# Kernel tuning notes

Measured on AMD Instinct MI355X. Metric: run time of the kernel, lower is better.

Reference implementation:

```python
import jax, jax.numpy as jnp
import numpy as np

N_INPUT, N_HIDDEN, N_LAYERS = 256, 1024, 3
BATCH, SEQ = 32, 512


def _uniform(key, shape, std):
    return jax.random.uniform(key, shape, jnp.float32, -std, std)


def setup_inputs() -> dict:
    key = jax.random.key(0)
    keys = jax.random.split(key, 32)
    std = 1.0 / float(np.sqrt(N_HIDDEN))
    inp = {"inputs": jax.random.normal(keys[0], (BATCH, SEQ, N_INPUT), jnp.float32)}
    ki = 1
    for l in range(N_LAYERS):
        d_in = N_INPUT if l == 0 else N_HIDDEN
        inp[f"Wxh{l}"] = _uniform(keys[ki], (3 * N_HIDDEN, d_in), std); ki += 1
        inp[f"bxh{l}"] = _uniform(keys[ki], (3 * N_HIDDEN,), std); ki += 1
        inp[f"Whh{l}"] = _uniform(keys[ki], (3 * N_HIDDEN, N_HIDDEN), std); ki += 1
        inp[f"bhh{l}"] = _uniform(keys[ki], (3 * N_HIDDEN,), std); ki += 1
        inp[f"Wnh{l}"] = _uniform(keys[ki], (3 * N_HIDDEN, N_INPUT), std); ki += 1
        inp[f"bnh{l}"] = _uniform(keys[ki], (3 * N_HIDDEN,), std); ki += 1
    inp["Wout"] = _uniform(keys[ki], (N_INPUT, N_HIDDEN), std); ki += 1
    inp["bout"] = _uniform(keys[ki], (N_INPUT,), std)
    return inp


def _moving_mean(x, s):
    # x: [T, B, D] -> sliding-window mean over time, window s, stride 1 -> [T-s+1, B, D]
    if s == 1:
        return x
    T = x.shape[0]
    return jnp.mean(jnp.stack([x[i:T - s + 1 + i] for i in range(s)], axis=0), axis=0)


def _gru_layer(xs, ms, h0, Wxh, bxh, Whh, bhh, Wnh, bnh):
    # xs, ms: [Tm, B, d] aligned per-timestep; h0: [B, H]
    # Precompute the time-parallel input/ms projections (batched GEMM).
    gx = jnp.einsum('tbd,gd->tbg', xs, Wxh) + bxh   # [Tm, B, 3H]
    gn = jnp.einsum('tbd,gd->tbg', ms, Wnh) + bnh   # [Tm, B, 3H]

    def step(h, g):
        gxt, gnt = g
        gh = h @ Whh.T + bhh
        i_r, i_i, i_n = jnp.split(gxt, 3, axis=-1)
        h_r, h_i, h_n = jnp.split(gh, 3, axis=-1)
        n_r, n_i, n_n = jnp.split(gnt, 3, axis=-1)
        resetgate = jax.nn.sigmoid(i_r + h_r + n_r)
        inputgate = jax.nn.sigmoid(i_i + h_i + n_i)
        newgate = jnp.tanh(i_n + resetgate * h_n + n_n)
        h_new = newgate + inputgate * (h - newgate)
        return h_new, h_new

    h_last, outs = jax.lax.scan(step, h0, (gx, gn))
    return outs, h_last


def reference(inputs,
              Wxh0, bxh0, Whh0, bhh0, Wnh0, bnh0,
              Wxh1, bxh1, Whh1, bhh1, Wnh1, bnh1,
              Wxh2, bxh2, Whh2, bhh2, Wnh2, bnh2,
              Wout, bout):
    params = [(Wxh0, bxh0, Whh0, bhh0, Wnh0, bnh0),
              (Wxh1, bxh1, Whh1, bhh1, Wnh1, bnh1),
              (Wxh2, bxh2, Whh2, bhh2, Wnh2, bnh2)]
    x = jnp.transpose(inputs, (1, 0, 2))  # batch_first -> [T, B, D]
    ms_list = [_moving_mean(x, 2 ** l) for l in range(N_LAYERS)]
    layer_in = x
    layers, hiddens = [], []
    for l in range(N_LAYERS):
        ms = ms_list[l]
        Tm = ms.shape[0]
        xs = layer_in[layer_in.shape[0] - Tm:]  # align tail of previous layer output
        h0 = jnp.zeros((x.shape[1], N_HIDDEN), dtype=x.dtype)
        outs, h_last = _gru_layer(xs, ms, h0, *params[l])
        layers.append(outs)
        hiddens.append(h_last)
        layer_in = outs
    layers = [jnp.einsum('tbh,oh->tbo', y, Wout) + bout for y in layers]
    return (*layers, *hiddens)
```

## Files before the change

### kernel.cpp

```cpp
#include <hip/hip_runtime.h>
#include <hip/hip_bf16.h>

typedef __bf16 bf16;
typedef __bf16 bf16x8 __attribute__((ext_vector_type(8)));
typedef float floatx4 __attribute__((ext_vector_type(4)));
typedef float floatx2 __attribute__((ext_vector_type(2)));
typedef unsigned int uint;
typedef uint uintx4 __attribute__((ext_vector_type(4)));
typedef unsigned long long u64;
typedef u64 u64x2 __attribute__((ext_vector_type(2)));
typedef __attribute__((address_space(1))) void gvoid;
typedef __attribute__((address_space(3))) void lvoid;

#define MFMA16(a, b, c) __builtin_amdgcn_mfma_f32_16x16x32_bf16((a), (b), (c), 0, 0, 0)
#define NB_REC 64
#define NB_W 64
#define FLAG_STRIDE 32
#define HSTR 1040
#define CHUNKF (32 * 32 * 3072)
#define AG __ATOMIC_RELAXED, __HIP_MEMORY_SCOPE_AGENT

struct MegaArgs {
    const bf16* xs[3];  int lda[3];
    const bf16* wXh[3]; int nkx[3];
    const bf16* ms[3];
    const bf16* wNh[3];
    const float* bxh[3]; const float* bnh[3];
    const float* Whh[3]; const float* bhh[3];
    bf16* outs[3];
    float* hid[3];
    float* G[3];
    uint* bar[3];
    uint* cdone[3];
    bf16* h01[3];
    int T[3];
};

static __device__ __forceinline__ floatx2 ldg2(const float* p) {
    union { u64 q; floatx2 f; } u;
    u.q = __hip_atomic_load((const u64*)p, AG);
    return u.f;
}

__global__ void k_cvt(const float* __restrict__ src, bf16* __restrict__ dst, int n) {
    int idx = blockIdx.x * 256 + threadIdx.x;
    if (idx < n) dst[idx] = (bf16)src[idx];
}

__global__ void k_prep(const float* __restrict__ inp, bf16* __restrict__ xT,
                       uint* __restrict__ bar) {
    size_t idx = (size_t)blockIdx.x * 256 + threadIdx.x;
    if (blockIdx.x == 0) {
        for (int i = threadIdx.x; i < 3 * NB_REC * FLAG_STRIDE + 64; i += 256)
            bar[i] = 0;
    }
    int d = (int)(idx & 255);
    int t = (int)((idx >> 8) & 511);
    int b = (int)(idx >> 17);
    xT[((size_t)(t * 32 + b) << 8) | d] = (bf16)inp[idx];
}

__global__ void k_movmean(const bf16* __restrict__ xT, bf16* __restrict__ out,
                          int s) {
    size_t idx = (size_t)blockIdx.x * 256 + threadIdx.x;
    int d = (int)(idx & 255);
    int m = (int)(idx >> 8);
    int t = m >> 5, b = m & 31;
    float acc = 0.f;
    for (int i = 0; i < s; ++i)
        acc += (float)xT[(((size_t)(t + i) * 32 + b) << 8) | d];
    out[idx] = (bf16)(acc * (1.f / (float)s));
}

__global__ __launch_bounds__(256, 2) void k_gemm(
    const bf16* __restrict__ A1, int lda1, const bf16* __restrict__ W1, int nk1,
    const bf16* __restrict__ A2, int lda2, const bf16* __restrict__ W2, int nk2,
    const float* __restrict__ bias1, const float* __restrict__ bias2,
    float* __restrict__ Cf, bf16* __restrict__ Cb, int ldc, int Mstore) {
    __shared__ bf16 lsA[128 * 64];
    __shared__ bf16 lsW[128 * 64];
    const int tid = threadIdx.x;
    const int lane = tid & 63, w = tid >> 6;
    const int quad = lane >> 4, lr = lane & 15;
    const int wm = w >> 1, wn = w & 1;
    const int m0 = blockIdx.y * 128, n0 = blockIdx.x * 128;

    floatx4 acc[4][4] = {};
    const bf16* As[2] = {A1, A2};
    const bf16* Ws[2] = {W1, W2};
    const int ldas[2] = {lda1, lda2};
    const int nks[2] = {nk1, nk2};

    for (int ph = 0; ph < 2; ++ph) {
        const int nk = nks[ph];
        if (nk == 0) continue;
        const bf16* A = As[ph];
        const bf16* Wp = Ws[ph];
        const int lda = ldas[ph];
        const int ldw = nk * 64;
        for (int kb = 0; kb < nk; ++kb) {
            const bf16* Ab = A + (size_t)m0 * lda + (size_t)kb * 64;
            const bf16* Wb = Wp + (size_t)n0 * ldw + (size_t)kb * 64;
#pragma unroll
            for (int i = 0; i < 4; ++i) {
                int c = (i * 4 + w) * 64 + lane;
                int m = c >> 3, q = c & 7;
                const bf16* g1 = Ab + (size_t)m * lda + ((q ^ (m & 7)) << 3);
                __builtin_amdgcn_global_load_lds((const gvoid*)g1,
                                                 (lvoid*)(lsA + (i * 4 + w) * 512), 16, 0, 0);
                const bf16* g2 = Wb + (size_t)m * ldw + ((q ^ (m & 7)) << 3);
                __builtin_amdgcn_global_load_lds((const gvoid*)g2,
                                                 (lvoid*)(lsW + (i * 4 + w) * 512), 16, 0, 0);
            }
            __syncthreads();
#pragma unroll
            for (int s = 0; s < 2; ++s) {
                bf16x8 af[4], bfr[4];
#pragma unroll
                for (int i = 0; i < 4; ++i) {
                    int kc = s * 4 + quad;
                    int m = wm * 64 + i * 16 + lr;
                    af[i] = *(const bf16x8*)(lsA + m * 64 + ((kc ^ (m & 7)) << 3));
                    int n = wn * 64 + i * 16 + lr;
                    bfr[i] = *(const bf16x8*)(lsW + n * 64 + ((kc ^ (n & 7)) << 3));
                }
#pragma unroll
                for (int i = 0; i < 4; ++i)
#pragma unroll
                    for (int j = 0; j < 4; ++j)
                        acc[i][j] = MFMA16(af[i], bfr[j], acc[i][j]);
            }
            __syncthreads();
        }
    }
#pragma unroll
    for (int j = 0; j < 4; ++j) {
        int col = n0 + wn * 64 + j * 16 + lr;
        float bs = 0.f;
        if (bias1) bs += bias1[col];
        if (bias2) bs += bias2[col];
#pragma unroll
        for (int i = 0; i < 4; ++i) {
            int rowb = m0 + wm * 64 + i * 16 + quad * 4;
#pragma unroll
            for (int r = 0; r < 4; ++r) {
                int row = rowb + r;
                if (row < Mstore) {
                    float v = acc[i][j][r] + bs;
                    if (Cf) Cf[(size_t)row * ldc + col] = v;
                    else    Cb[(size_t)row * ldc + col] = (bf16)v;
                }
            }
        }
    }
}

__global__ __launch_bounds__(384, 1) void k_rec(
    const float* __restrict__ G, const float* __restrict__ Whh,
    const float* __restrict__ bhh, bf16* __restrict__ outs,
    bf16* __restrict__ h01, float* __restrict__ hf,
    float* __restrict__ hid_out, uint* __restrict__ bar,
    int T, int init, int final_, uint tgt0) {
    const int tid = threadIdx.x, blk = blockIdx.x;
    const int lane = tid & 63, w = tid >> 6;
    const int quad = lane >> 4, lr = lane & 15;
    const int mi = (w >= 3) ? 1 : 0, ni = w - mi * 3;

    __shared__ __attribute__((aligned(16))) char smem[73088];
    bf16* hT = (bf16*)smem;
    float* gh = (float*)(smem + 66560);

    const float* wrow = Whh + ((size_t)ni * 1024 + blk * 16 + lr) * 1024 + quad * 8;
    bf16x8 breg[32];
#pragma unroll
    for (int kt = 0; kt < 32; ++kt) {
        const floatx4* p = (const floatx4*)(wrow + kt * 32);
        floatx4 lo = p[0], hi = p[1];
        bf16x8 b;
        b[0] = (bf16)lo.x; b[1] = (bf16)lo.y; b[2] = (bf16)lo.z; b[3] = (bf16)lo.w;
        b[4] = (bf16)hi.x; b[5] = (bf16)hi.y; b[6] = (bf16)hi.z; b[7] = (bf16)hi.w;
        breg[kt] = b;
    }

    const int eb = tid >> 3;
    const int ec = (tid & 7) * 2;
    const int ecg = blk * 16 + ec;

    float bhr0 = 0.f, bhr1 = 0.f, bhi0 = 0.f, bhi1 = 0.f, bhn0 = 0.f, bhn1 = 0.f;
    float hreg0 = 0.f, hreg1 = 0.f;
    if (tid < 256) {
        bhr0 = bhh[ecg];        bhr1 = bhh[ecg + 1];
        bhi0 = bhh[1024 + ecg]; bhi1 = bhh[1024 + ecg + 1];
        bhn0 = bhh[2048 + ecg]; bhn1 = bhh[2048 + ecg + 1];
        if (!init) {
            floatx2 h = *(const floatx2*)(hf + (size_t)eb * 1024 + ecg);
            hreg0 = h.x;
            hreg1 = h.y;
        }
        union { bf16 h[2]; uint u; } pk;
        pk.h[0] = (bf16)hreg0;
        pk.h[1] = (bf16)hreg1;
        __hip_atomic_store((uint*)(h01 + (size_t)eb * 1024 + ecg), pk.u, AG);
    }

    floatx2 pAr, pAi, pAn, pBr, pBi, pBn;
    if (tid < 256) {
        const float* Grow = G + (size_t)eb * 3072 + ecg;
        pAr = *(const floatx2*)(Grow);
        pAi = *(const floatx2*)(Grow + 1024);
        pAn = *(const floatx2*)(Grow + 2048);
    }

    uint* myflag = bar + (uint)blk * FLAG_STRIDE;

    __syncthreads();
    if (tid == 0) __hip_atomic_store(myflag, tgt0, AG);
    if (tid < NB_REC) {
        const uint* fp = bar + (uint)tid * FLAG_STRIDE;
        while (__hip_atomic_load(fp, AG) < tgt0) __builtin_amdgcn_s_sleep(1);
    }
    __syncthreads();

    for (int t = 0; t < T; ++t) {
        const bf16* hb = h01 + (size_t)(t & 1) * (32 * 1024);
        bf16* hn = h01 + (size_t)((t + 1) & 1) * (32 * 1024);

        u64 s0[11], s1[11];
#pragma unroll
        for (int r = 0; r < 11; ++r) {
            int ci = tid + r * 384;
            if (r < 10 || ci < 4096) {
                const u64* src = (const u64*)(hb + (size_t)ci * 8);
                s0[r] = __hip_atomic_load(src, AG);
                s1[r] = __hip_atomic_load(src + 1, AG);
            }
        }
#pragma unroll
        for (int r = 0; r < 11; ++r) {
            int ci = tid + r * 384;
            if (r < 10 || ci < 4096) {
                int row = ci >> 7, q = ci & 127;
                u64x2 v; v.x = s0[r]; v.y = s1[r];
                *(u64x2*)(hT + row * HSTR + q * 8) = v;
            }
        }
        __syncthreads();

        floatx4 acc0 = {0.f, 0.f, 0.f, 0.f}, acc1 = {0.f, 0.f, 0.f, 0.f};
        const bf16* aB = hT + (mi * 16 + lr) * HSTR + quad * 8;
#pragma unroll
        for (int kt = 0; kt < 32; kt += 2) {
            bf16x8 a0 = *(const bf16x8*)(aB + kt * 32);
            acc0 = MFMA16(a0, breg[kt], acc0);
            bf16x8 a1 = *(const bf16x8*)(aB + kt * 32 + 32);
            acc1 = MFMA16(a1, breg[kt + 1], acc1);
        }
        floatx4 acc = acc0 + acc1;
#pragma unroll
        for (int r = 0; r < 4; ++r)
            gh[(ni * 32 + mi * 16 + quad * 4 + r) * 17 + lr] = acc[r];
        __syncthreads();

        uint pku = 0u;
        if (tid < 256) {
            float ghr0 = gh[eb * 17 + ec]            + bhr0;
            float ghr1 = gh[eb * 17 + ec + 1]        + bhr1;
            float ghi0 = gh[(32 + eb) * 17 + ec]     + bhi0;
            float ghi1 = gh[(32 + eb) * 17 + ec + 1] + bhi1;
            float ghn0 = gh[(64 + eb) * 17 + ec]     + bhn0;
            float ghn1 = gh[(64 + eb) * 17 + ec + 1] + bhn1;
            float rg0 = 1.f / (1.f + __expf(-(pAr.x + ghr0)));
            float rg1 = 1.f / (1.f + __expf(-(pAr.y + ghr1)));
            float ig0 = 1.f / (1.f + __expf(-(pAi.x + ghi0)));
            float ig1 = 1.f / (1.f + __expf(-(pAi.y + ghi1)));
            float pre0 = pAn.x + rg0 * ghn0;
            float pre1 = pAn.y + rg1 * ghn1;
            float e20 = __expf(2.f * pre0);
            float e21 = __expf(2.f * pre1);
            float ng0 = 1.f - 2.f / (e20 + 1.f);
            float ng1 = 1.f - 2.f / (e21 + 1.f);
            hreg0 = ng0 + ig0 * (hreg0 - ng0);
            hreg1 = ng1 + ig1 * (hreg1 - ng1);
            union { bf16 h[2]; uint u; } pk;
            pk.h[0] = (bf16)hreg0;
            pk.h[1] = (bf16)hreg1;
            pku = pk.u;
            __hip_atomic_store((uint*)(hn + (size_t)eb * 1024 + ecg), pku, AG);
        }
        __syncthreads();

        uint tgt = tgt0 + 1 + (uint)t;
        if (tid == 0) __hip_atomic_store(myflag, tgt, AG);

        if (tid < 256) {
            if (t + 1 < T) {
                const float* Grow = G + ((size_t)(t + 1) * 32 + eb) * 3072 + ecg;
                pBr = *(const floatx2*)(Grow);
                pBi = *(const floatx2*)(Grow + 1024);
                pBn = *(const floatx2*)(Grow + 2048);
            }
            *(uint*)(outs + ((size_t)t * 32 + eb) * 1024 + ecg) = pku;
        }
        if (t + 1 < T && tid < NB_REC) {
            const uint* fp = bar + (uint)tid * FLAG_STRIDE;
            while (__hip_atomic_load(fp, AG) < tgt) __builtin_amdgcn_s_sleep(1);
        }
        __syncthreads();

        pAr = pBr; pAi = pBi; pAn = pBn;
    }

    if (tid < 256) {
        floatx2 h; h.x = hreg0; h.y = hreg1;
        *(floatx2*)(hf + (size_t)eb * 1024 + ecg) = h;
        if (final_) *(floatx2*)(hid_out + (size_t)eb * 1024 + ecg) = h;
    }
}

__global__ __launch_bounds__(384, 1) void k_mega(MegaArgs A) {
    __shared__ __attribute__((aligned(16))) char smem[98304];
    const int tid = threadIdx.x, blk = blockIdx.x;
    const int lane = tid & 63, w = tid >> 6;
    const int quad = lane >> 4, lr = lane & 15;

    if (blk >= 192) {
        bf16* lsA = (bf16*)smem;
        bf16* lsW = (bf16*)(smem + 16384);
        const int wid = blk - 192;
        const int wr = w / 3, wc = w - wr * 3;
        for (int key = 0; key <= 36; ++key) {
            for (int l = 0; l < 3; ++l) {
                int rem = key - 3 * l;
                if (rem < 0 || (rem & 1)) continue;
                int c = rem >> 1;
                if (c >= 16) continue;
                if (l > 0) {
                    uint need = (uint)((c + 1) * 32 + l + 1);
                    uint cap = (uint)(A.T[l - 1] + 2);
                    if (need > cap) need = cap;
                    if (tid < 64) {
                        const uint* fp = A.bar[l - 1] + (uint)tid * FLAG_STRIDE;
                        while (__hip_atomic_load(fp, AG) < need)
                            __builtin_amdgcn_s_sleep(2);
                    }
                }
                if (c >= 2) {
                    uint need = (uint)((c - 1) * 32);
                    if (tid < 64) {
                        const uint* fp = A.bar[l] + (uint)tid * FLAG_STRIDE;
                        while (__hip_atomic_load(fp, AG) < need)
                            __builtin_amdgcn_s_sleep(2);
                    }
                }
                __syncthreads();
                const bf16* xsP = A.xs[l];
                const bf16* msP = A.ms[l];
                const bf16* wxP = A.wXh[l];
                const bf16* wnP = A.wNh[l];
                const float* b1 = A.bxh[l];
                const float* b2 = A.bnh[l];
                float* Gs = A.G[l] + (size_t)(c & 1) * CHUNKF;
                const int Mst = A.T[l] * 32;
                const int nks[2] = {A.nkx[l], 4};
                const bf16* Aps[2] = {xsP, msP};
                const int ldas[2] = {A.lda[l], 256};
                const bf16* Wps[2] = {wxP, wnP};
#pragma unroll 1
                for (int half = 0; half < 2; ++half) {
                    int tl = wid * 2 + half;
                    int by = tl >> 4, bx = tl & 15;
                    int m0g = c * 1024 + by * 128;
                    int n0 = bx * 192;
                    floatx4 acc[4][4] = {};
                    for (int ph = 0; ph < 2; ++ph) {
                        const int nk = nks[ph];
                        const bf16* Ap = Aps[ph];
                        const int ldap = ldas[ph];
                        const bf16* Wp = Wps[ph];
                        const int ldw = nk * 64;
                        for (int kb = 0; kb < nk; ++kb) {
                            const bf16* Ab = Ap + (size_t)m0g * ldap + (size_t)kb * 64;
                            const bf16* Wb = Wp + (size_t)n0 * ldw + (size_t)kb * 64;
#pragma unroll
                            for (int r = 0; r < 7; ++r) {
                                int idx = tid + r * 384;
                                if (r < 6 || idx < 2560) {
                                    if (idx < 1024) {
                                        int m = idx >> 3, q = idx & 7;
                                        const bf16* src = Ab + (size_t)m * ldap + ((q ^ (m & 7)) << 3);
                                        __builtin_amdgcn_global_load_lds(
                                            (const gvoid*)src, (lvoid*)(lsA + idx * 8), 16, 0, 0);
                                    } else {
                                        int j2 = idx - 1024;
                                        int m = j2 >> 3, q = j2 & 7;
                                        const bf16* src = Wb + (size_t)m * ldw + ((q ^ (m & 7)) << 3);
                                        __builtin_amdgcn_global_load_lds(
                                            (const gvoid*)src, (lvoid*)(lsW + j2 * 8), 16, 0, 0);
                                    }
                                }
                            }
                            __syncthreads();
#pragma unroll
                            for (int s = 0; s < 2; ++s) {
                                bf16x8 af[4], bfr[4];
#pragma unroll
                                for (int i = 0; i < 4; ++i) {
                                    int kc = s * 4 + quad;
                                    int mA = wr * 64 + i * 16 + lr;
                                    af[i] = *(const bf16x8*)(lsA + mA * 64 + ((kc ^ (mA & 7)) << 3));
                                    int nB = wc * 64 + i * 16 + lr;
                                    bfr[i] = *(const bf16x8*)(lsW + nB * 64 + ((kc ^ (nB & 7)) << 3));
                                }
#pragma unroll
                                for (int i = 0; i < 4; ++i)
#pragma unroll
                                    for (int j = 0; j < 4; ++j)
                                        acc[i][j] = MFMA16(af[i], bfr[j], acc[i][j]);
                            }
                            __syncthreads();
                        }
                    }
#pragma unroll
                    for (int j = 0; j < 4; ++j) {
                        int col = n0 + wc * 64 + j * 16 + lr;
                        float bs = b1[col] + b2[col];
#pragma unroll
                        for (int i = 0; i < 4; ++i) {
                            int rowb = m0g + wr * 64 + i * 16 + quad * 4;
#pragma unroll
                            for (int r = 0; r < 4; ++r) {
                                int row = rowb + r;
                                if (row < Mst) {
                                    float v = acc[i][j][r] + bs;
                                    __hip_atomic_store(
                                        (uint*)(Gs + (size_t)(row - c * 1024) * 3072 + col),
                                        __float_as_uint(v), AG);
                                }
                            }
                        }
                    }
                }
                __syncthreads();
                if (tid == 0) atomicAdd(A.cdone[l] + c, 1u);
            }
        }
        return;
    }

    const int l = blk >> 6, cs = blk & 63;
    const int T = A.T[l];
    bf16* hT = (bf16*)smem;
    float* gh = (float*)(smem + 66560);
    const int mi = (w >= 3) ? 1 : 0, ni = w - mi * 3;

    const float* Whh = A.Whh[l];
    const float* bhh = A.bhh[l];
    bf16* outs = A.outs[l];
    bf16* h01 = A.h01[l];
    float* Gb = A.G[l];
    uint* bar = A.bar[l];
    const uint* cdone = A.cdone[l];

    const float* wrow = Whh + ((size_t)ni * 1024 + cs * 16 + lr) * 1024 + quad * 8;
    bf16x8 breg[32];
#pragma unroll
    for (int kt = 0; kt < 32; ++kt) {
        const floatx4* p = (const floatx4*)(wrow + kt * 32);
        floatx4 lo = p[0], hi = p[1];
        bf16x8 b;
        b[0] = (bf16)lo.x; b[1] = (bf16)lo.y; b[2] = (bf16)lo.z; b[3] = (bf16)lo.w;
        b[4] = (bf16)hi.x; b[5] = (bf16)hi.y; b[6] = (bf16)hi.z; b[7] = (bf16)hi.w;
        breg[kt] = b;
    }

    const int eb = tid >> 3;
    const int ec = (tid & 7) * 2;
    const int ecg = cs * 16 + ec;

    float bhr0 = 0.f, bhr1 = 0.f, bhi0 = 0.f, bhi1 = 0.f, bhn0 = 0.f, bhn1 = 0.f;
    if (tid < 256) {
        bhr0 = bhh[ecg];        bhr1 = bhh[ecg + 1];
        bhi0 = bhh[1024 + ecg]; bhi1 = bhh[1024 + ecg + 1];
        bhn0 = bhh[2048 + ecg]; bhn1 = bhh[2048 + ecg + 1];
    }
    float hreg0 = 0.f, hreg1 = 0.f;
    floatx2 pAr = {0.f, 0.f}, pAi = {0.f, 0.f}, pAn = {0.f, 0.f};
    floatx2 pBr = {0.f, 0.f}, pBi = {0.f, 0.f}, pBn = {0.f, 0.f};
    uint* myflag = bar + (uint)cs * FLAG_STRIDE;

    for (int t = 0; t < T; ++t) {
        if ((t & 31) == 0) {
            const uint* cd = cdone + (t >> 5);
            if (tid < 64) {
                while (__hip_atomic_load(cd, AG) < (uint)NB_W)
                    __builtin_amdgcn_s_sleep(1);
            }
            __syncthreads();
            if (tid < 256) {
                const float* Grow = Gb + (size_t)((t >> 5) & 1) * CHUNKF
                                      + ((size_t)(t & 31) * 32 + eb) * 3072 + ecg;
                pAr = ldg2(Grow);
                pAi = ldg2(Grow + 1024);
                pAn = ldg2(Grow + 2048);
            }
        }

        if (t == 0) {
            for (int i = tid; i < 4096; i += 384) {
                int row = i >> 7, q = i & 127;
                uintx4 z = {0u, 0u, 0u, 0u};
                *(uintx4*)(hT + row * HSTR + q * 8) = z;
            }
        } else {
            const bf16* hb = h01 + (size_t)(t & 1) * (32 * 1024);
            u64 s0[11], s1[11];
#pragma unroll
            for (int r = 0; r < 11; ++r) {
                int ci = tid + r * 384;
                if (r < 10 || ci < 4096) {
                    const u64* src = (const u64*)(hb + (size_t)ci * 8);
                    s0[r] = __hip_atomic_load(src, AG);
                    s1[r] = __hip_atomic_load(src + 1, AG);
                }
            }
#pragma unroll
            for (int r = 0; r < 11; ++r) {
                int ci = tid + r * 384;
                if (r < 10 || ci < 4096) {
                    int row = ci >> 7, q = ci & 127;
                    u64x2 v; v.x = s0[r]; v.y = s1[r];
                    *(u64x2*)(hT + row * HSTR + q * 8) = v;
                }
            }
        }
        __syncthreads();

        floatx4 acc0 = {0.f, 0.f, 0.f, 0.f}, acc1 = {0.f, 0.f, 0.f, 0.f};
        const bf16* aB = hT + (mi * 16 + lr) * HSTR + quad * 8;
#pragma unroll
        for (int kt = 0; kt < 32; kt += 2) {
            bf16x8 a0 = *(const bf16x8*)(aB + kt * 32);
            acc0 = MFMA16(a0, breg[kt], acc0);
            bf16x8 a1 = *(const bf16x8*)(aB + kt * 32 + 32);
            acc1 = MFMA16(a1, breg[kt + 1], acc1);
        }
        floatx4 acc = acc0 + acc1;
#pragma unroll
        for (int r = 0; r < 4; ++r)
            gh[(ni * 32 + mi * 16 + quad * 4 + r) * 17 + lr] = acc[r];
        __syncthreads();

        uint pku = 0u;
        if (tid < 256) {
            float ghr0 = gh[eb * 17 + ec]            + bhr0;
            float ghr1 = gh[eb * 17 + ec + 1]        + bhr1;
            float ghi0 = gh[(32 + eb) * 17 + ec]     + bhi0;
            float ghi1 = gh[(32 + eb) * 17 + ec + 1] + bhi1;
            float ghn0 = gh[(64 + eb) * 17 + ec]     + bhn0;
            float ghn1 = gh[(64 + eb) * 17 + ec + 1] + bhn1;
            float rg0 = 1.f / (1.f + __expf(-(pAr.x + ghr0)));
            float rg1 = 1.f / (1.f + __expf(-(pAr.y + ghr1)));
            float ig0 = 1.f / (1.f + __expf(-(pAi.x + ghi0)));
            float ig1 = 1.f / (1.f + __expf(-(pAi.y + ghi1)));
            float pre0 = pAn.x + rg0 * ghn0;
            float pre1 = pAn.y + rg1 * ghn1;
            float e20 = __expf(2.f * pre0);
            float e21 = __expf(2.f * pre1);
            float ng0 = 1.f - 2.f / (e20 + 1.f);
            float ng1 = 1.f - 2.f / (e21 + 1.f);
            hreg0 = ng0 + ig0 * (hreg0 - ng0);
            hreg1 = ng1 + ig1 * (hreg1 - ng1);
            union { bf16 h[2]; uint u; } pk;
            pk.h[0] = (bf16)hreg0;
            pk.h[1] = (bf16)hreg1;
            pku = pk.u;
            __hip_atomic_store((uint*)(h01 + (size_t)((t + 1) & 1) * (32 * 1024)
                                       + (size_t)eb * 1024 + ecg), pku, AG);
        }
        __syncthreads();

        if (tid == 0) __hip_atomic_store(myflag, (uint)(t + 1), AG);

        if (tid < 256) {
            if (t + 1 < T && ((t + 1) & 31) != 0) {
                const float* Grow = Gb + (size_t)((t >> 5) & 1) * CHUNKF
                                      + ((size_t)((t + 1) & 31) * 32 + eb) * 3072 + ecg;
                pBr = ldg2(Grow);
                pBi = ldg2(Grow + 1024);
                pBn = ldg2(Grow + 2048);
            }
            __hip_atomic_store((uint*)(outs + ((size_t)t * 32 + eb) * 1024 + ecg),
                               pku, AG);
        }
        if (t + 1 < T && tid < 64) {
            const uint* fp = bar + (uint)tid * FLAG_STRIDE;
            while (__hip_atomic_load(fp, AG) < (uint)(t + 1))
                __builtin_amdgcn_s_sleep(1);
        }
        __syncthreads();

        pAr = pBr; pAi = pBi; pAn = pBn;
    }

    if (tid == 0) __hip_atomic_store(myflag, (uint)(T + 2), AG);
    if (tid < 256) {
        floatx2 h; h.x = hreg0; h.y = hreg1;
        *(floatx2*)(A.hid[l] + (size_t)eb * 1024 + ecg) = h;
    }
}

extern "C" void kernel_launch(void* const* d_in, const int* in_sizes, int n_in,
                              void* d_out, int out_size, void* d_ws, size_t ws_size,
                              hipStream_t stream) {
    const float* inp  = (const float*)d_in[0];
    const float* Wxh0 = (const float*)d_in[1];
    const float* bxh0 = (const float*)d_in[2];
    const float* Whh0 = (const float*)d_in[3];
    const float* bhh0 = (const float*)d_in[4];
    const float* Wnh0 = (const float*)d_in[5];
    const float* bnh0 = (const float*)d_in[6];
    const float* Wxh1 = (const float*)d_in[7];
    const float* bxh1 = (const float*)d_in[8];
    const float* Whh1 = (const float*)d_in[9];
    const float* bhh1 = (const float*)d_in[10];
    const float* Wnh1 = (const float*)d_in[11];
    const float* bnh1 = (const float*)d_in[12];
    const float* Wxh2 = (const float*)d_in[13];
    const float* bxh2 = (const float*)d_in[14];
    const float* Whh2 = (const float*)d_in[15];
    const float* bhh2 = (const float*)d_in[16];
    const float* Wnh2 = (const float*)d_in[17];
    const float* bnh2 = (const float*)d_in[18];
    const float* Wout = (const float*)d_in[19];
    const float* bout = (const float*)d_in[20];
    float* out = (float*)d_out;

    char* ws = (char*)d_ws;
    size_t o = 0;
    auto take = [&](size_t bytes) {
        o = (o + 255) & ~(size_t)255;
        char* p = ws + o;
        o += bytes;
        return p;
    };
    const size_t RP = 16512;
    bf16* xT    = (bf16*)take(RP * 256 * 2);
    bf16* ms1   = (bf16*)take(RP * 256 * 2);
    bf16* ms2   = (bf16*)take(RP * 256 * 2);
    bf16* outs0 = (bf16*)take(RP * 1024 * 2);
    bf16* outs1 = (bf16*)take(RP * 1024 * 2);
    bf16* outs2 = (bf16*)take(RP * 1024 * 2);
    bf16* h01   = (bf16*)take((size_t)3 * 2 * 32 * 1024 * 2);
    float* hf   = (float*)take((size_t)32 * 1024 * 4);
    uint* bar   = (uint*)take((size_t)(3 * NB_REC * FLAG_STRIDE + 64) * 4);
    bf16* wXh0 = (bf16*)take((size_t)3072 * 256 * 2);
    bf16* wXh1 = (bf16*)take((size_t)3072 * 1024 * 2);
    bf16* wXh2 = (bf16*)take((size_t)3072 * 1024 * 2);
    bf16* wNh0 = (bf16*)take((size_t)3072 * 256 * 2);
    bf16* wNh1 = (bf16*)take((size_t)3072 * 256 * 2);
    bf16* wNh2 = (bf16*)take((size_t)3072 * 256 * 2);
    bf16* wOut = (bf16*)take((size_t)256 * 1024 * 2);
    o = (o + 255) & ~(size_t)255;
    float* G = (float*)(ws + o);
    size_t availG = (ws_size > o) ? (ws_size - o) : 0;
    const int use_mega = availG >= (size_t)6 * CHUNKF * 4;
    (void)in_sizes; (void)n_in; (void)out_size;

    const size_t o0 = 0, o1 = (size_t)512 * 32 * 256, o2 = o1 + (size_t)511 * 32 * 256;
    const size_t ohid = o2 + (size_t)509 * 32 * 256;

    auto cvt = [&](const float* s, bf16* d, int n) {
        k_cvt<<<(n + 255) / 256, 256, 0, stream>>>(s, d, n);
    };
    cvt(Wout, wOut, 256 * 1024);
    cvt(Wxh0, wXh0, 3072 * 256);
    cvt(Wxh1, wXh1, 3072 * 1024);
    cvt(Wxh2, wXh2, 3072 * 1024);
    cvt(Wnh0, wNh0, 3072 * 256);
    cvt(Wnh1, wNh1, 3072 * 256);
    cvt(Wnh2, wNh2, 3072 * 256);
    k_prep<<<16384, 256, 0, stream>>>(inp, xT, bar);
    k_movmean<<<511 * 32, 256, 0, stream>>>(xT, ms1, 2);
    k_movmean<<<509 * 32, 256, 0, stream>>>(xT, ms2, 4);

    if (use_mega) {
        MegaArgs A;
        const bf16* xsA[3]  = {xT, outs0 + (size_t)32 * 1024, outs1 + (size_t)64 * 1024};
        const int ldaA[3]   = {256, 1024, 1024};
        const bf16* wXhA[3] = {wXh0, wXh1, wXh2};
        const int nkxA[3]   = {4, 16, 16};
        const bf16* msA[3]  = {xT, ms1, ms2};
        const bf16* wNhA[3] = {wNh0, wNh1, wNh2};
        const float* bxhA[3] = {bxh0, bxh1, bxh2};
        const float* bnhA[3] = {bnh0, bnh1, bnh2};
        const float* WhhA[3] = {Whh0, Whh1, Whh2};
        const float* bhhA[3] = {bhh0, bhh1, bhh2};
        bf16* outsA[3] = {outs0, outs1, outs2};
        const int TA[3] = {512, 511, 509};
        for (int l = 0; l < 3; ++l) {
            A.xs[l] = xsA[l];   A.lda[l] = ldaA[l];
            A.wXh[l] = wXhA[l]; A.nkx[l] = nkxA[l];
            A.ms[l] = msA[l];   A.wNh[l] = wNhA[l];
            A.bxh[l] = bxhA[l]; A.bnh[l] = bnhA[l];
            A.Whh[l] = WhhA[l]; A.bhh[l] = bhhA[l];
            A.outs[l] = outsA[l];
            A.hid[l] = out + ohid + (size_t)l * 32768;
            A.G[l] = G + (size_t)l * 2 * CHUNKF;
            A.bar[l] = bar + (size_t)l * NB_REC * FLAG_STRIDE;
            A.cdone[l] = bar + 3 * NB_REC * FLAG_STRIDE + 16 * l;
            A.h01[l] = h01 + (size_t)l * 2 * 32 * 1024;
            A.T[l] = TA[l];
        }
        k_mega<<<256, 384, 0, stream>>>(A);
    } else {
        int CT = (int)(availG / ((size_t)32 * 3072 * 4));
        if (CT > 512) CT = 512;
        if (CT < 4) CT = 4;
        auto run_layer = [&](const bf16* xs, int ldx, const bf16* wXh, int nkx,
                             const bf16* ms, const bf16* wNh,
                             const float* bxh, const float* bnh,
                             const float* Whh, const float* bhh,
                             bf16* outs, float* hid, int T, int layer) {
            uint base = 0;
            for (int t0 = 0; t0 < T; t0 += CT) {
                int ct = (T - t0 < CT) ? (T - t0) : CT;
                int gy = (ct * 32 + 127) / 128;
                k_gemm<<<dim3(24, gy), 256, 0, stream>>>(
                    xs + (size_t)t0 * 32 * ldx, ldx, wXh, nkx,
                    ms + (size_t)t0 * 32 * 256, 256, wNh, 4,
                    bxh, bnh, G, (bf16*)nullptr, 3072, ct * 32);
                k_rec<<<NB_REC, 384, 0, stream>>>(
                    G, Whh, bhh, outs + (size_t)t0 * 32 * 1024, h01, hf, hid,
                    bar + (size_t)NB_REC * FLAG_STRIDE * layer, ct,
                    (t0 == 0) ? 1 : 0, (t0 + ct >= T) ? 1 : 0, base + 1);
                base += (uint)ct + 1;
            }
        };
        run_layer(xT, 256, wXh0, 4, xT, wNh0, bxh0, bnh0, Whh0, bhh0,
                  outs0, out + ohid, 512, 0);
        run_layer(outs0 + (size_t)32 * 1024, 1024, wXh1, 16, ms1, wNh1,
                  bxh1, bnh1, Whh1, bhh1, outs1, out + ohid + 32768, 511, 1);
        run_layer(outs1 + (size_t)64 * 1024, 1024, wXh2, 16, ms2, wNh2,
                  bxh2, bnh2, Whh2, bhh2, outs2, out + ohid + 65536, 509, 2);
    }

    k_gemm<<<dim3(2, 128), 256, 0, stream>>>(outs0, 1024, wOut, 16,
                                             nullptr, 0, nullptr, 0, bout, nullptr,
                                             out + o0, nullptr, 256, 16384);
    k_gemm<<<dim3(2, 128), 256, 0, stream>>>(outs1, 1024, wOut, 16,
                                             nullptr, 0, nullptr, 0, bout, nullptr,
                                             out + o1, nullptr, 256, 16352);
    k_gemm<<<dim3(2, 128), 256, 0, stream>>>(outs2, 1024, wOut, 16,
                                             nullptr, 0, nullptr, 0, bout, nullptr,
                                             out + o2, nullptr, 256, 16288);
}
```

Measured before the change: 2.870 ms.

## Halve recurrent blocks per layer with 768-thread blocks, merge GEMM halves

The persistent mega kernel now uses 32 recurrent blocks per layer instead of 64. Each block has 768 threads and owns 32 hidden columns, which halves the number of blocks taking part in the per-timestep flag barrier. The GEMM worker blocks also go to 768 threads and compute their two tiles concurrently, one per half-block with separate LDS buffers, instead of one after the other. The cost is fewer, larger blocks: per-thread register pressure is capped by the 768-thread launch bound, and each block does more work on the serial recurrence path.

Result: slower. 4.933 ms (+71.9%).

```diff
diff --git a/kernel.cpp b/kernel.cpp
--- a/kernel.cpp
+++ b/kernel.cpp
@@ -14,6 +14,7 @@
 
 #define MFMA16(a, b, c) __builtin_amdgcn_mfma_f32_16x16x32_bf16((a), (b), (c), 0, 0, 0)
 #define NB_REC 64
+#define NB_RECL 32
 #define NB_W 64
 #define FLAG_STRIDE 32
 #define HSTR 1040
@@ -317,17 +318,20 @@
     }
 }
 
-__global__ __launch_bounds__(384, 1) void k_mega(MegaArgs A) {
+__global__ __launch_bounds__(768, 1) void k_mega(MegaArgs A) {
     __shared__ __attribute__((aligned(16))) char smem[98304];
     const int tid = threadIdx.x, blk = blockIdx.x;
     const int lane = tid & 63, w = tid >> 6;
     const int quad = lane >> 4, lr = lane & 15;
 
-    if (blk >= 192) {
-        bf16* lsA = (bf16*)smem;
-        bf16* lsW = (bf16*)(smem + 16384);
-        const int wid = blk - 192;
-        const int wr = w / 3, wc = w - wr * 3;
+    if (blk >= 3 * NB_RECL) {
+        const int wid = blk - 3 * NB_RECL;
+        const int half = (tid >= 384) ? 1 : 0;
+        const int tidh = tid - half * 384;
+        const int wh = tidh >> 6;
+        const int wr = wh / 3, wc = wh - wr * 3;
+        bf16* lsA = (bf16*)(smem + half * 40960);
+        bf16* lsW = (bf16*)(smem + half * 40960 + 16384);
         for (int key = 0; key <= 36; ++key) {
             for (int l = 0; l < 3; ++l) {
                 int rem = key - 3 * l;
@@ -338,7 +342,7 @@
                     uint need = (uint)((c + 1) * 32 + l + 1);
                     uint cap = (uint)(A.T[l - 1] + 2);
                     if (need > cap) need = cap;
-                    if (tid < 64) {
+                    if (tid < NB_RECL) {
                         const uint* fp = A.bar[l - 1] + (uint)tid * FLAG_STRIDE;
                         while (__hip_atomic_load(fp, AG) < need)
                             __builtin_amdgcn_s_sleep(2);
@@ -346,96 +350,89 @@
                 }
                 if (c >= 2) {
                     uint need = (uint)((c - 1) * 32);
-                    if (tid < 64) {
+                    if (tid < NB_RECL) {
                         const uint* fp = A.bar[l] + (uint)tid * FLAG_STRIDE;
                         while (__hip_atomic_load(fp, AG) < need)
                             __builtin_amdgcn_s_sleep(2);
                     }
                 }
                 __syncthreads();
-                const bf16* xsP = A.xs[l];
-                const bf16* msP = A.ms[l];
-                const bf16* wxP = A.wXh[l];
-                const bf16* wnP = A.wNh[l];
-                const float* b1 = A.bxh[l];
-                const float* b2 = A.bnh[l];
                 float* Gs = A.G[l] + (size_t)(c & 1) * CHUNKF;
                 const int Mst = A.T[l] * 32;
                 const int nks[2] = {A.nkx[l], 4};
-                const bf16* Aps[2] = {xsP, msP};
+                const bf16* Aps[2] = {A.xs[l], A.ms[l]};
                 const int ldas[2] = {A.lda[l], 256};
-                const bf16* Wps[2] = {wxP, wnP};
-#pragma unroll 1
-                for (int half = 0; half < 2; ++half) {
-                    int tl = wid * 2 + half;
-                    int by = tl >> 4, bx = tl & 15;
-                    int m0g = c * 1024 + by * 128;
-                    int n0 = bx * 192;
-                    floatx4 acc[4][4] = {};
-                    for (int ph = 0; ph < 2; ++ph) {
-                        const int nk = nks[ph];
-                        const bf16* Ap = Aps[ph];
-                        const int ldap = ldas[ph];
-                        const bf16* Wp = Wps[ph];
-                        const int ldw = nk * 64;
-                        for (int kb = 0; kb < nk; ++kb) {
-                            const bf16* Ab = Ap + (size_t)m0g * ldap + (size_t)kb * 64;
-                            const bf16* Wb = Wp + (size_t)n0 * ldw + (size_t)kb * 64;
-#pragma unroll
-                            for (int r = 0; r < 7; ++r) {
-                                int idx = tid + r * 384;
-                                if (r < 6 || idx < 2560) {
-                                    if (idx < 1024) {
-                                        int m = idx >> 3, q = idx & 7;
-                                        const bf16* src = Ab + (size_t)m * ldap + ((q ^ (m & 7)) << 3);
-                                        __builtin_amdgcn_global_load_lds(
-                                            (const gvoid*)src, (lvoid*)(lsA + idx * 8), 16, 0, 0);
-                                    } else {
-                                        int j2 = idx - 1024;
-                                        int m = j2 >> 3, q = j2 & 7;
-                                        const bf16* src = Wb + (size_t)m * ldw + ((q ^ (m & 7)) << 3);
-                                        __builtin_amdgcn_global_load_lds(
-                                            (const gvoid*)src, (lvoid*)(lsW + j2 * 8), 16, 0, 0);
-                                    }
+                const bf16* Wps[2] = {A.wXh[l], A.wNh[l]};
+                const float* b1 = A.bxh[l];
+                const float* b2 = A.bnh[l];
+                int tl = wid * 2 + half;
+                int by = tl >> 4, bx = tl & 15;
+                int m0g = c * 1024 + by * 128;
+                int n0 = bx * 192;
+                floatx4 acc[4][4] = {};
+                for (int ph = 0; ph < 2; ++ph) {
+                    const int nk = nks[ph];
+                    const bf16* Ap = Aps[ph];
+                    const int ldap = ldas[ph];
+                    const bf16* Wp = Wps[ph];
+                    const int ldw = nk * 64;
+                    for (int kb = 0; kb < nk; ++kb) {
+                        const bf16* Ab = Ap + (size_t)m0g * ldap + (size_t)kb * 64;
+                        const bf16* Wb = Wp + (size_t)n0 * ldw + (size_t)kb * 64;
+#pragma unroll
+                        for (int r = 0; r < 7; ++r) {
+                            int idx = tidh + r * 384;
+                            if (r < 6 || idx < 2560) {
+                                if (idx < 1024) {
+                                    int m = idx >> 3, q = idx & 7;
+                                    const bf16* src = Ab + (size_t)m * ldap + ((q ^ (m & 7)) << 3);
+                                    __builtin_amdgcn_global_load_lds(
+                                        (const gvoid*)src, (lvoid*)(lsA + idx * 8), 16, 0, 0);
+                                } else {
+                                    int j2 = idx - 1024;
+                                    int m = j2 >> 3, q = j2 & 7;
+                                    const bf16* src = Wb + (size_t)m * ldw + ((q ^ (m & 7)) << 3);
+                                    __builtin_amdgcn_global_load_lds(
+                                        (const gvoid*)src, (lvoid*)(lsW + j2 * 8), 16, 0, 0);
                                 }
                             }
-                            __syncthreads();
-#pragma unroll
-                            for (int s = 0; s < 2; ++s) {
-                                bf16x8 af[4], bfr[4];
-#pragma unroll
-                                for (int i = 0; i < 4; ++i) {
-                                    int kc = s * 4 + quad;
-                                    int mA = wr * 64 + i * 16 + lr;
-                                    af[i] = *(const bf16x8*)(lsA + mA * 64 + ((kc ^ (mA & 7)) << 3));
-                                    int nB = wc * 64 + i * 16 + lr;
-                                    bfr[i] = *(const bf16x8*)(lsW + nB * 64 + ((kc ^ (nB & 7)) << 3));
-                                }
-#pragma unroll
-                                for (int i = 0; i < 4; ++i)
-#pragma unroll
-                                    for (int j = 0; j < 4; ++j)
-                                        acc[i][j] = MFMA16(af[i], bfr[j], acc[i][j]);
+                        }
+                        __syncthreads();
+#pragma unroll
+                        for (int s = 0; s < 2; ++s) {
+                            bf16x8 af[4], bfr[4];
+#pragma unroll
+                            for (int i = 0; i < 4; ++i) {
+                                int kc = s * 4 + quad;
+                                int mA = wr * 64 + i * 16 + lr;
+                                af[i] = *(const bf16x8*)(lsA + mA * 64 + ((kc ^ (mA & 7)) << 3));
+                                int nB = wc * 64 + i * 16 + lr;
+                                bfr[i] = *(const bf16x8*)(lsW + nB * 64 + ((kc ^ (nB & 7)) << 3));
                             }
-                            __syncthreads();
+#pragma unroll
+                            for (int i = 0; i < 4; ++i)
+#pragma unroll
+                                for (int j = 0; j < 4; ++j)
+                                    acc[i][j] = MFMA16(af[i], bfr[j], acc[i][j]);
                         }
+                        __syncthreads();
                     }
-#pragma unroll
-                    for (int j = 0; j < 4; ++j) {
-                        int col = n0 + wc * 64 + j * 16 + lr;
-                        float bs = b1[col] + b2[col];
-#pragma unroll
-                        for (int i = 0; i < 4; ++i) {
-                            int rowb = m0g + wr * 64 + i * 16 + quad * 4;
-#pragma unroll
-                            for (int r = 0; r < 4; ++r) {
-                                int row = rowb + r;
-                                if (row < Mst) {
-                                    float v = acc[i][j][r] + bs;
-                                    __hip_atomic_store(
-                                        (uint*)(Gs + (size_t)(row - c * 1024) * 3072 + col),
-                                        __float_as_uint(v), AG);
-                                }
+                }
+#pragma unroll
+                for (int j = 0; j < 4; ++j) {
+                    int col = n0 + wc * 64 + j * 16 + lr;
+                    float bs = b1[col] + b2[col];
+#pragma unroll
+                    for (int i = 0; i < 4; ++i) {
+                        int rowb = m0g + wr * 64 + i * 16 + quad * 4;
+#pragma unroll
+                        for (int r = 0; r < 4; ++r) {
+                            int row = rowb + r;
+                            if (row < Mst) {
+                                float v = acc[i][j][r] + bs;
+                                __hip_atomic_store(
+                                    (uint*)(Gs + (size_t)(row - c * 1024) * 3072 + col),
+                                    __float_as_uint(v), AG);
                             }
                         }
                     }
@@ -447,11 +444,13 @@
         return;
     }
 
-    const int l = blk >> 6, cs = blk & 63;
+    const int l = blk >> 5, cs = blk & 31;
     const int T = A.T[l];
     bf16* hT = (bf16*)smem;
     float* gh = (float*)(smem + 66560);
-    const int mi = (w >= 3) ? 1 : 0, ni = w - mi * 3;
+    const int mi = (w >= 6) ? 1 : 0;
+    const int u = w - mi * 6;
+    const int g = u % 3, q = u / 3;
 
     const float* Whh = A.Whh[l];
     const float* bhh = A.bhh[l];
@@ -461,7 +460,7 @@
     uint* bar = A.bar[l];
     const uint* cdone = A.cdone[l];
 
-    const float* wrow = Whh + ((size_t)ni * 1024 + cs * 16 + lr) * 1024 + quad * 8;
+    const float* wrow = Whh + ((size_t)g * 1024 + cs * 32 + q * 16 + lr) * 1024 + quad * 8;
     bf16x8 breg[32];
 #pragma unroll
     for (int kt = 0; kt < 32; ++kt) {
@@ -473,12 +472,12 @@
         breg[kt] = b;
     }
 
-    const int eb = tid >> 3;
-    const int ec = (tid & 7) * 2;
-    const int ecg = cs * 16 + ec;
+    const int eb = tid >> 4;
+    const int ec = (tid & 15) * 2;
+    const int ecg = cs * 32 + ec;
 
     float bhr0 = 0.f, bhr1 = 0.f, bhi0 = 0.f, bhi1 = 0.f, bhn0 = 0.f, bhn1 = 0.f;
-    if (tid < 256) {
+    if (tid < 512) {
         bhr0 = bhh[ecg];        bhr1 = bhh[ecg + 1];
         bhi0 = bhh[1024 + ecg]; bhi1 = bhh[1024 + ecg + 1];
         bhn0 = bhh[2048 + ecg]; bhn1 = bhh[2048 + ecg + 1];
@@ -496,7 +495,7 @@
                     __builtin_amdgcn_s_sleep(1);
             }
             __syncthreads();
-            if (tid < 256) {
+            if (tid < 512) {
                 const float* Grow = Gb + (size_t)((t >> 5) & 1) * CHUNKF
                                       + ((size_t)(t & 31) * 32 + eb) * 3072 + ecg;
                 pAr = ldg2(Grow);
@@ -506,30 +505,30 @@
         }
 
         if (t == 0) {
-            for (int i = tid; i < 4096; i += 384) {
-                int row = i >> 7, q = i & 127;
+            for (int i = tid; i < 4096; i += 768) {
+                int row = i >> 7, qq = i & 127;
                 uintx4 z = {0u, 0u, 0u, 0u};
-                *(uintx4*)(hT + row * HSTR + q * 8) = z;
+                *(uintx4*)(hT + row * HSTR + qq * 8) = z;
             }
         } else {
             const bf16* hb = h01 + (size_t)(t & 1) * (32 * 1024);
-            u64 s0[11], s1[11];
-#pragma unroll
-            for (int r = 0; r < 11; ++r) {
-                int ci = tid + r * 384;
-                if (r < 10 || ci < 4096) {
+            u64 s0[6], s1[6];
+#pragma unroll
+            for (int r = 0; r < 6; ++r) {
+                int ci = tid + r * 768;
+                if (r < 5 || ci < 4096) {
                     const u64* src = (const u64*)(hb + (size_t)ci * 8);
                     s0[r] = __hip_atomic_load(src, AG);
                     s1[r] = __hip_atomic_load(src + 1, AG);
                 }
             }
 #pragma unroll
-            for (int r = 0; r < 11; ++r) {
-                int ci = tid + r * 384;
-                if (r < 10 || ci < 4096) {
-                    int row = ci >> 7, q = ci & 127;
+            for (int r = 0; r < 6; ++r) {
+                int ci = tid + r * 768;
+                if (r < 5 || ci < 4096) {
+                    int row = ci >> 7, qq = ci & 127;
                     u64x2 v; v.x = s0[r]; v.y = s1[r];
-                    *(u64x2*)(hT + row * HSTR + q * 8) = v;
+                    *(u64x2*)(hT + row * HSTR + qq * 8) = v;
                 }
             }
         }
@@ -547,17 +546,17 @@
         floatx4 acc = acc0 + acc1;
 #pragma unroll
         for (int r = 0; r < 4; ++r)
-            gh[(ni * 32 + mi * 16 + quad * 4 + r) * 17 + lr] = acc[r];
+            gh[(g * 32 + mi * 16 + quad * 4 + r) * 33 + q * 16 + lr] = acc[r];
         __syncthreads();
 
         uint pku = 0u;
-        if (tid < 256) {
-            float ghr0 = gh[eb * 17 + ec]            + bhr0;
-            float ghr1 = gh[eb * 17 + ec + 1]        + bhr1;
-            float ghi0 = gh[(32 + eb) * 17 + ec]     + bhi0;
-            float ghi1 = gh[(32 + eb) * 17 + ec + 1] + bhi1;
-            float ghn0 = gh[(64 + eb) * 17 + ec]     + bhn0;
-            float ghn1 = gh[(64 + eb) * 17 + ec + 1] + bhn1;
+        if (tid < 512) {
+            float ghr0 = gh[eb * 33 + ec]            + bhr0;
+            float ghr1 = gh[eb * 33 + ec + 1]        + bhr1;
+            float ghi0 = gh[(32 + eb) * 33 + ec]     + bhi0;
+            float ghi1 = gh[(32 + eb) * 33 + ec + 1] + bhi1;
+            float ghn0 = gh[(64 + eb) * 33 + ec]     + bhn0;
+            float ghn1 = gh[(64 + eb) * 33 + ec + 1] + bhn1;
             float rg0 = 1.f / (1.f + __expf(-(pAr.x + ghr0)));
             float rg1 = 1.f / (1.f + __expf(-(pAr.y + ghr1)));
             float ig0 = 1.f / (1.f + __expf(-(pAi.x + ghi0)));
@@ -581,7 +580,7 @@
 
         if (tid == 0) __hip_atomic_store(myflag, (uint)(t + 1), AG);
 
-        if (tid < 256) {
+        if (tid < 512) {
             if (t + 1 < T && ((t + 1) & 31) != 0) {
                 const float* Grow = Gb + (size_t)((t >> 5) & 1) * CHUNKF
                                       + ((size_t)((t + 1) & 31) * 32 + eb) * 3072 + ecg;
@@ -592,7 +591,7 @@
             __hip_atomic_store((uint*)(outs + ((size_t)t * 32 + eb) * 1024 + ecg),
                                pku, AG);
         }
-        if (t + 1 < T && tid < 64) {
+        if (t + 1 < T && tid < NB_RECL) {
             const uint* fp = bar + (uint)tid * FLAG_STRIDE;
             while (__hip_atomic_load(fp, AG) < (uint)(t + 1))
                 __builtin_amdgcn_s_sleep(1);
@@ -603,7 +602,7 @@
     }
 
     if (tid == 0) __hip_atomic_store(myflag, (uint)(T + 2), AG);
-    if (tid < 256) {
+    if (tid < 512) {
         floatx2 h; h.x = hreg0; h.y = hreg1;
         *(floatx2*)(A.hid[l] + (size_t)eb * 1024 + ecg) = h;
     }
@@ -706,12 +705,12 @@
             A.outs[l] = outsA[l];
             A.hid[l] = out + ohid + (size_t)l * 32768;
             A.G[l] = G + (size_t)l * 2 * CHUNKF;
-            A.bar[l] = bar + (size_t)l * NB_REC * FLAG_STRIDE;
+            A.bar[l] = bar + (size_t)l * NB_RECL * FLAG_STRIDE;
             A.cdone[l] = bar + 3 * NB_REC * FLAG_STRIDE + 16 * l;
             A.h01[l] = h01 + (size_t)l * 2 * 32 * 1024;
             A.T[l] = TA[l];
         }
-        k_mega<<<256, 384, 0, stream>>>(A);
+        k_mega<<<3 * NB_RECL + NB_W, 768, 0, stream>>>(A);
     } else {
         int CT = (int)(availG / ((size_t)32 * 3072 * 4));
         if (CT > 512) CT = 512;
```
